# Performance work log

Measured on AMD Instinct MI355X. Metric: run time of the kernel, lower is better.

## Reference

```python
import jax, jax.numpy as jnp
import numpy as np

H = 512

def setup_inputs() -> dict:
    key = jax.random.key(0)
    ks = jax.random.split(key, 8)
    s = 1.0 / np.sqrt(H)
    return {
        "encoder_outputs": jax.random.normal(ks[0], (64, 2048, H), dtype=jnp.float32),
        "decoder_hidden": jax.random.normal(ks[1], (64, H), dtype=jnp.float32),
        "W1": jax.random.uniform(ks[2], (H, H), jnp.float32, -s, s),
        "b1": jax.random.uniform(ks[3], (H,), jnp.float32, -s, s),
        "W2": jax.random.uniform(ks[4], (H, H), jnp.float32, -s, s),
        "b2": jax.random.uniform(ks[5], (H,), jnp.float32, -s, s),
        "V": jax.random.uniform(ks[6], (H,), jnp.float32, -s, s),  # V weight (1, H) squeezed
        "bv": jax.random.uniform(ks[7], (1,), jnp.float32, -s, s),
    }

def reference(encoder_outputs, decoder_hidden, W1, b1, W2, b2, V, bv):
    # proj of encoder outputs: [B,S,H]; proj of decoder hidden: [B,1,H]
    enc_proj = jnp.einsum('bsh,oh->bso', encoder_outputs, W1) + b1
    dec_proj = (jnp.einsum('bh,oh->bo', decoder_hidden, W2) + b2)[:, None, :]
    energy = jnp.tanh(enc_proj + dec_proj)                      # [B,S,H]
    scores = jnp.einsum('bsh,h->bs', energy, V) + bv[0]          # [B,S]
    attn = jax.nn.softmax(scores, axis=1)                        # [B,S]
    context = jnp.einsum('bs,bsh->bh', attn, encoder_outputs)    # [B,H]
    return context, attn
```

## Files before the change

### kernel.cpp

```cpp
#include <hip/hip_runtime.h>
#include <hip/hip_bf16.h>

typedef __attribute__((ext_vector_type(4))) float f32x4;
typedef __attribute__((ext_vector_type(8))) short s16x8;
typedef __attribute__((ext_vector_type(4))) unsigned short u16x4;
typedef __attribute__((ext_vector_type(8))) __bf16 bf16x8;

#define HDIM 512
#define SEQ  2048
#define NB   64
#define BM   64
#define NBLK ((NB * SEQ) / BM)
#define CPB  (SEQ / BM)

static __device__ __forceinline__ unsigned short f2bf(float f) {
  unsigned u = __float_as_uint(f);
  u += 0x7fffu + ((u >> 16) & 1u);
  return (unsigned short)(u >> 16);
}
static __device__ __forceinline__ float bf2f(unsigned short v) {
  return __uint_as_float(((unsigned)v) << 16);
}

static __device__ __forceinline__ f32x4 mfma16(s16x8 a, s16x8 b, f32x4 c) {
  return __builtin_amdgcn_mfma_f32_16x16x32_bf16(
      __builtin_bit_cast(bf16x8, a), __builtin_bit_cast(bf16x8, b), c, 0, 0, 0);
}

#define BLOADG(dst, sp)                                                        \
  do {                                                                         \
    asm volatile("global_load_dwordx4 %0, %1, %2 offset:0"                     \
                 : "=&v"((dst)[0]) : "v"(voff), "s"(sp));                      \
    asm volatile("global_load_dwordx4 %0, %1, %2 offset:1024"                  \
                 : "=&v"((dst)[1]) : "v"(voff), "s"(sp));                      \
    asm volatile("global_load_dwordx4 %0, %1, %2 offset:2048"                  \
                 : "=&v"((dst)[2]) : "v"(voff), "s"(sp));                      \
    asm volatile("global_load_dwordx4 %0, %1, %2 offset:3072"                  \
                 : "=&v"((dst)[3]) : "v"(voff), "s"(sp));                      \
  } while (0)

__global__ void convert_w1(const float* __restrict__ w1,
                           unsigned short* __restrict__ o) {
  int id = blockIdx.x * 256 + threadIdx.x;
  int kk = id >> 11, n = (id >> 2) & 511, r4 = id & 3;
  const float* src = w1 + (long)n * HDIM + kk * 32 + r4 * 8;
  f32x4 v0 = *(const f32x4*)src;
  f32x4 v1 = *(const f32x4*)(src + 4);
  u16x4 a, b;
  a.x = f2bf(v0.x); a.y = f2bf(v0.y); a.z = f2bf(v0.z); a.w = f2bf(v0.w);
  b.x = f2bf(v1.x); b.y = f2bf(v1.y); b.z = f2bf(v1.z); b.w = f2bf(v1.w);
  unsigned short* dst = o + (long)id * 8;
  *(u16x4*)dst = a;
  *(u16x4*)(dst + 4) = b;
}

__global__ void zproj(const float* __restrict__ dec, const float* __restrict__ W2,
                      const float* __restrict__ b1, const float* __restrict__ b2,
                      float* __restrict__ zfull) {
  int b = blockIdx.x, oc = blockIdx.y, tid = threadIdx.x;
  int o = oc * 256 + tid;
  __shared__ float d_s[HDIM];
  d_s[tid] = dec[b * HDIM + tid];
  d_s[tid + 256] = dec[b * HDIM + tid + 256];
  __syncthreads();
  const float* w = W2 + (long)o * HDIM;
  float s = 0.f;
#pragma unroll 4
  for (int k = 0; k < HDIM; k += 4) {
    f32x4 v = *(const f32x4*)(w + k);
    s += v.x * d_s[k] + v.y * d_s[k + 1] + v.z * d_s[k + 2] + v.w * d_s[k + 3];
  }
  zfull[b * HDIM + o] = s + b1[o] + b2[o];
}

__global__ __launch_bounds__(512, 4)
void gemm_fused(const float* __restrict__ enc, const unsigned short* __restrict__ w1k,
                const float* __restrict__ zfull, const float* __restrict__ V,
                const float* __restrict__ bv, float* __restrict__ scores,
                unsigned short* __restrict__ pctx, float* __restrict__ ml) {
  __shared__ __align__(16) char pool[71936];
  unsigned short* Asm = (unsigned short*)pool;
  float* zbuf = (float*)(pool + 65536);
  float* vbuf = (float*)(pool + 67584);
  float* red  = (float*)(pool + 69632);
  float* plds = (float*)(pool + 71680);
  float* pcr  = (float*)pool;

  const int tid = threadIdx.x;
  const int wid = tid >> 6;
  const int lane = tid & 63;
  const long m0 = (long)blockIdx.x * BM;
  const int b = (int)(m0 >> 11);

  zbuf[tid] = zfull[b * HDIM + tid];
  vbuf[tid] = V[tid];

  {
    const float* Ablk = enc + m0 * HDIM;
    const int qf32 = tid & 127;
    const int rbase = tid >> 7;
    const int q = qf32 >> 1, half = qf32 & 1;
#pragma unroll
    for (int j = 0; j < 16; ++j) {
      const int row = j * 4 + rbase;
      f32x4 v = *(const f32x4*)(Ablk + (long)row * HDIM + qf32 * 4);
      u16x4 pk;
      pk.x = f2bf(v.x); pk.y = f2bf(v.y); pk.z = f2bf(v.z); pk.w = f2bf(v.w);
      *(u16x4*)((char*)Asm + row * 1024 + ((q ^ (row & 7)) * 16) + half * 8) = pk;
    }
  }

  const int r4 = lane >> 4, c15 = lane & 15, c7 = c15 & 7;
  const char* Ab = (const char*)Asm;
  const unsigned voff = (unsigned)((wid * 64 + c15) * 64 + r4 * 16);
  const int widu = __builtin_amdgcn_readfirstlane(wid);

  f32x4 acc[4][4] = {};
  s16x8 bX[4], bY[4];

  __syncthreads();

  BLOADG(bX, w1k + ((widu & 15) * 16384));

#pragma unroll
  for (int kk = 0; kk < 16; ++kk) {
    const int ke = (kk + widu) & 15;
    s16x8* cur = (kk & 1) ? bY : bX;
    s16x8* nxt = (kk & 1) ? bX : bY;

    s16x8 af[4];
    const int abase = c15 * 1024 + (((ke * 4 + r4) ^ c7) * 16);
#pragma unroll
    for (int mf = 0; mf < 4; ++mf)
      af[mf] = *(const s16x8*)(Ab + abase + mf * 16384);

    if (kk < 15) {
      const unsigned short* sp = w1k + ((((kk + 1) + widu) & 15) * 16384);
      BLOADG(nxt, sp);
      asm volatile("s_waitcnt vmcnt(4)");
    } else {
      asm volatile("s_waitcnt vmcnt(0)");
    }
    __builtin_amdgcn_sched_barrier(0);

#pragma unroll
    for (int mf = 0; mf < 4; ++mf)
#pragma unroll
      for (int nf = 0; nf < 4; ++nf)
        acc[mf][nf] = mfma16(af[mf], cur[nf], acc[mf][nf]);
  }

  float zr[4], vr[4];
#pragma unroll
  for (int nf = 0; nf < 4; ++nf) {
    const int n = wid * 64 + nf * 16 + c15;
    zr[nf] = zbuf[n];
    vr[nf] = vbuf[n];
  }
#pragma unroll
  for (int mf = 0; mf < 4; ++mf) {
#pragma unroll
    for (int j = 0; j < 4; ++j) {
      float s = 0.f;
#pragma unroll
      for (int nf = 0; nf < 4; ++nf) {
        float x = acc[mf][nf][j] + zr[nf];
        float e = __expf(2.f * x);
        float t = 1.f - 2.f * __builtin_amdgcn_rcpf(e + 1.f);
        s += t * vr[nf];
      }
      s += __shfl_xor(s, 1); s += __shfl_xor(s, 2);
      s += __shfl_xor(s, 4); s += __shfl_xor(s, 8);
      if (c15 == 0) red[wid * BM + mf * 16 + r4 * 4 + j] = s;
    }
  }
  __syncthreads();

  if (tid < BM) {
    float s = 0.f;
#pragma unroll
    for (int w = 0; w < 8; ++w) s += red[w * BM + tid];
    s += bv[0];
    scores[m0 + tid] = s;
    float mc = s;
#pragma unroll
    for (int off = 1; off < 64; off <<= 1) mc = fmaxf(mc, __shfl_xor(mc, off));
    float p = __expf(s - mc);
    plds[tid] = p;
    float lc = p;
#pragma unroll
    for (int off = 1; off < 64; off <<= 1) lc += __shfl_xor(lc, off);
    if (tid == 0) { ml[blockIdx.x * 2] = mc; ml[blockIdx.x * 2 + 1] = lc; }
  }
  __syncthreads();

  float c8[8] = {};
#pragma unroll
  for (int rr = 0; rr < 8; ++rr) {
    const int r = wid * 8 + rr;
    s16x8 v = *(const s16x8*)(Ab + r * 1024 + ((lane ^ rr) * 16));
    const float p = plds[r];
#pragma unroll
    for (int e = 0; e < 8; ++e)
      c8[e] += p * bf2f((unsigned short)v[e]);
  }
  __syncthreads();
  {
    f32x4 w0, w1;
    w0.x = c8[0]; w0.y = c8[1]; w0.z = c8[2]; w0.w = c8[3];
    w1.x = c8[4]; w1.y = c8[5]; w1.z = c8[6]; w1.w = c8[7];
    *(f32x4*)((char*)pcr + wid * 2048 + lane * 32) = w0;
    *(f32x4*)((char*)pcr + wid * 2048 + lane * 32 + 16) = w1;
  }
  __syncthreads();
  {
    float s = 0.f;
#pragma unroll
    for (int g = 0; g < 8; ++g) s += pcr[g * 512 + tid];
    pctx[(long)blockIdx.x * HDIM + tid] = f2bf(s);
  }
}

__global__ void combine(float* __restrict__ attn, const unsigned short* __restrict__ pctx,
                        const float* __restrict__ ml, float* __restrict__ ctx) {
  const int b = blockIdx.x, tid = threadIdx.x;
  const int lane = tid & 63;
  float m = -1e30f, l = 0.f;
  if (lane < CPB) {
    m = ml[(b * CPB + lane) * 2];
    l = ml[(b * CPB + lane) * 2 + 1];
  }
  float M = m;
#pragma unroll
  for (int off = 1; off < 64; off <<= 1) M = fmaxf(M, __shfl_xor(M, off));
  float le = (lane < CPB) ? l * __expf(m - M) : 0.f;
  float L = le;
#pragma unroll
  for (int off = 1; off < 64; off <<= 1) L += __shfl_xor(L, off);
  const float invL = 1.f / L;

  __shared__ float wc[CPB];
  if (tid < CPB) wc[tid] = __expf(ml[(b * CPB + tid) * 2] - M) * invL;

  float sv[4];
#pragma unroll
  for (int i = 0; i < 4; ++i) sv[i] = attn[(long)b * SEQ + i * 512 + tid];
#pragma unroll
  for (int i = 0; i < 4; ++i)
    attn[(long)b * SEQ + i * 512 + tid] = __expf(sv[i] - M) * invL;

  __syncthreads();
  float a = 0.f;
#pragma unroll 8
  for (int c = 0; c < CPB; ++c)
    a += bf2f(pctx[(long)(b * CPB + c) * HDIM + tid]) * wc[c];
  ctx[(long)b * HDIM + tid] = a;
}

extern "C" void kernel_launch(void* const* d_in, const int* in_sizes, int n_in,
                              void* d_out, int out_size, void* d_ws, size_t ws_size,
                              hipStream_t stream) {
  const float* enc = (const float*)d_in[0];
  const float* dec = (const float*)d_in[1];
  const float* W1  = (const float*)d_in[2];
  const float* b1  = (const float*)d_in[3];
  const float* W2  = (const float*)d_in[4];
  const float* b2  = (const float*)d_in[5];
  const float* V   = (const float*)d_in[6];
  const float* bv  = (const float*)d_in[7];

  float* out  = (float*)d_out;
  float* ctx  = out;
  float* attn = out + NB * HDIM;

  char* ws = (char*)d_ws;
  unsigned short* w1k  = (unsigned short*)ws;
  float*          zful = (float*)(ws + 524288);
  unsigned short* pctx = (unsigned short*)(ws + 655360);
  float*          mlb  = (float*)(ws + 2752512);
  (void)in_sizes; (void)n_in; (void)out_size; (void)ws_size;

  convert_w1<<<128, 256, 0, stream>>>(W1, w1k);
  zproj<<<dim3(NB, 2), 256, 0, stream>>>(dec, W2, b1, b2, zful);
  gemm_fused<<<NBLK, 512, 0, stream>>>(enc, w1k, zful, V, bv, attn, pctx, mlb);
  combine<<<NB, 512, 0, stream>>>(attn, pctx, mlb, ctx);
}
```

Baseline: 123.9 us.

## Stream encoder tile into LDS per k-slice, overlapped with W1 loads and MFMA

The block no longer loads and converts the whole 64x512 encoder tile to bf16 in LDS before the GEMM starts. It preloads three k-slices, then inside the k-loop issues global loads for slice kk+4 alongside the W1 fragment loads and packs slice kk+3 into LDS, with a barrier each iteration. This hides the encoder-tile load latency behind MFMA work. It also drops the per-wave staggered k order, raises wave priority around the MFMA section, and adds a workgroup barrier on every k-step.

```diff
diff --git a/kernel.cpp b/kernel.cpp
--- a/kernel.cpp
+++ b/kernel.cpp
@@ -37,6 +37,19 @@
                  : "=&v"((dst)[2]) : "v"(voff), "s"(sp));                      \
     asm volatile("global_load_dwordx4 %0, %1, %2 offset:3072"                  \
                  : "=&v"((dst)[3]) : "v"(voff), "s"(sp));                      \
+  } while (0)
+
+#define SLOAD(dst, s)                                                          \
+  asm volatile("global_load_dwordx4 %0, %1, %2"                                \
+               : "=&v"(dst) : "v"(aoff), "s"(encblk + (s) * 32))
+
+#define PACKW(src, s)                                                          \
+  do {                                                                         \
+    u16x4 pk;                                                                  \
+    pk.x = f2bf((src).x); pk.y = f2bf((src).y);                                \
+    pk.z = f2bf((src).z); pk.w = f2bf((src).w);                                \
+    *(u16x4*)((char*)Asm + wrow * 1024 +                                       \
+              (((((s) * 4) + (wc >> 1)) ^ wr7) * 16) + (wc & 1) * 8) = pk;     \
   } while (0)
 
 __global__ void convert_w1(const float* __restrict__ w1,
@@ -95,59 +108,64 @@
   zbuf[tid] = zfull[b * HDIM + tid];
   vbuf[tid] = V[tid];
 
-  {
-    const float* Ablk = enc + m0 * HDIM;
-    const int qf32 = tid & 127;
-    const int rbase = tid >> 7;
-    const int q = qf32 >> 1, half = qf32 & 1;
-#pragma unroll
-    for (int j = 0; j < 16; ++j) {
-      const int row = j * 4 + rbase;
-      f32x4 v = *(const f32x4*)(Ablk + (long)row * HDIM + qf32 * 4);
-      u16x4 pk;
-      pk.x = f2bf(v.x); pk.y = f2bf(v.y); pk.z = f2bf(v.z); pk.w = f2bf(v.w);
-      *(u16x4*)((char*)Asm + row * 1024 + ((q ^ (row & 7)) * 16) + half * 8) = pk;
-    }
-  }
-
   const int r4 = lane >> 4, c15 = lane & 15, c7 = c15 & 7;
   const char* Ab = (const char*)Asm;
   const unsigned voff = (unsigned)((wid * 64 + c15) * 64 + r4 * 16);
-  const int widu = __builtin_amdgcn_readfirstlane(wid);
+
+  const int wrow = tid >> 3, wc = tid & 7, wr7 = wrow & 7;
+  const float* encblk = enc + m0 * HDIM;
+  const unsigned aoff = (unsigned)(wrow * 2048 + wc * 16);
+
+  {
+    const float* ep = encblk + (long)wrow * HDIM + wc * 4;
+#pragma unroll
+    for (int s = 0; s < 3; ++s) {
+      f32x4 v = *(const f32x4*)(ep + s * 32);
+      PACKW(v, s);
+    }
+  }
+  __syncthreads();
 
   f32x4 acc[4][4] = {};
   s16x8 bX[4], bY[4];
-
-  __syncthreads();
-
-  BLOADG(bX, w1k + ((widu & 15) * 16384));
+  f32x4 sb0, sb1;
+
+  SLOAD(sb1, 3);
+  BLOADG(bX, w1k);
 
 #pragma unroll
   for (int kk = 0; kk < 16; ++kk) {
-    const int ke = (kk + widu) & 15;
-    s16x8* cur = (kk & 1) ? bY : bX;
-    s16x8* nxt = (kk & 1) ? bX : bY;
-
-    s16x8 af[4];
-    const int abase = c15 * 1024 + (((ke * 4 + r4) ^ c7) * 16);
-#pragma unroll
-    for (int mf = 0; mf < 4; ++mf)
-      af[mf] = *(const s16x8*)(Ab + abase + mf * 16384);
-
-    if (kk < 15) {
-      const unsigned short* sp = w1k + ((((kk + 1) + widu) & 15) * 16384);
-      BLOADG(nxt, sp);
-      asm volatile("s_waitcnt vmcnt(4)");
-    } else {
-      asm volatile("s_waitcnt vmcnt(0)");
-    }
+    if (kk <= 11) {
+      if (kk & 1) SLOAD(sb1, kk + 4); else SLOAD(sb0, kk + 4);
+    }
+    if (kk <= 14) {
+      const unsigned short* sp = w1k + (kk + 1) * 16384;
+      if (kk & 1) BLOADG(bX, sp); else BLOADG(bY, sp);
+    }
+    if (kk <= 11)      asm volatile("s_waitcnt vmcnt(5)" ::: "memory");
+    else if (kk <= 14) asm volatile("s_waitcnt vmcnt(4)" ::: "memory");
+    else               asm volatile("s_waitcnt vmcnt(0)" ::: "memory");
     __builtin_amdgcn_sched_barrier(0);
-
-#pragma unroll
-    for (int mf = 0; mf < 4; ++mf)
-#pragma unroll
-      for (int nf = 0; nf < 4; ++nf)
-        acc[mf][nf] = mfma16(af[mf], cur[nf], acc[mf][nf]);
+    if (kk <= 12) {
+      if (kk & 1) PACKW(sb0, kk + 3); else PACKW(sb1, kk + 3);
+    }
+    asm volatile("s_waitcnt lgkmcnt(0)" ::: "memory");
+    __builtin_amdgcn_s_barrier();
+    __builtin_amdgcn_sched_barrier(0);
+    const int abase = c15 * 1024 + (((kk * 4 + r4) ^ c7) * 16);
+    __builtin_amdgcn_s_setprio(1);
+#pragma unroll
+    for (int mf = 0; mf < 4; ++mf) {
+      s16x8 af = *(const s16x8*)(Ab + abase + mf * 16384);
+      if (kk & 1) {
+#pragma unroll
+        for (int nf = 0; nf < 4; ++nf) acc[mf][nf] = mfma16(af, bY[nf], acc[mf][nf]);
+      } else {
+#pragma unroll
+        for (int nf = 0; nf < 4; ++nf) acc[mf][nf] = mfma16(af, bX[nf], acc[mf][nf]);
+      }
+    }
+    __builtin_amdgcn_s_setprio(0);
   }
 
   float zr[4], vr[4];
```

Measured after the change: 125.0 us. Within noise of the previous version (+0.9%).

## Merge prep kernels, pipeline A-tile staging, and split MFMA waits per B fragment

Applied to the files above, without the earlier changes.

Combines the W1 conversion and decoder projection into one launch to save a kernel launch. The encoder tile staging now issues batches of inline-asm global loads and overlaps them with bf16 packing into shared memory, instead of doing loads and packs in sequence. The main loop waits for each B fragment separately, so MFMAs on early fragments can start before the later loads land, and it raises wave priority around the MFMA section. The z and V vectors are now read straight from global memory instead of staged LDS buffers, which shrinks LDS use but adds scattered global reads in the epilogue.

```diff
diff --git a/kernel.cpp b/kernel.cpp
--- a/kernel.cpp
+++ b/kernel.cpp
@@ -39,38 +39,59 @@
                  : "=&v"((dst)[3]) : "v"(voff), "s"(sp));                      \
   } while (0)
 
-__global__ void convert_w1(const float* __restrict__ w1,
-                           unsigned short* __restrict__ o) {
-  int id = blockIdx.x * 256 + threadIdx.x;
-  int kk = id >> 11, n = (id >> 2) & 511, r4 = id & 3;
-  const float* src = w1 + (long)n * HDIM + kk * 32 + r4 * 8;
-  f32x4 v0 = *(const f32x4*)src;
-  f32x4 v1 = *(const f32x4*)(src + 4);
-  u16x4 a, b;
-  a.x = f2bf(v0.x); a.y = f2bf(v0.y); a.z = f2bf(v0.z); a.w = f2bf(v0.w);
-  b.x = f2bf(v1.x); b.y = f2bf(v1.y); b.z = f2bf(v1.z); b.w = f2bf(v1.w);
-  unsigned short* dst = o + (long)id * 8;
-  *(u16x4*)dst = a;
-  *(u16x4*)(dst + 4) = b;
-}
-
-__global__ void zproj(const float* __restrict__ dec, const float* __restrict__ W2,
-                      const float* __restrict__ b1, const float* __restrict__ b2,
-                      float* __restrict__ zfull) {
-  int b = blockIdx.x, oc = blockIdx.y, tid = threadIdx.x;
-  int o = oc * 256 + tid;
-  __shared__ float d_s[HDIM];
-  d_s[tid] = dec[b * HDIM + tid];
-  d_s[tid + 256] = dec[b * HDIM + tid + 256];
-  __syncthreads();
-  const float* w = W2 + (long)o * HDIM;
-  float s = 0.f;
+#define SLOAD(dst, s)                                                          \
+  asm volatile("global_load_dwordx4 %0, %1, %2"                                \
+               : "=&v"(dst) : "v"(aoff), "s"(encblk + (s) * 32))
+
+#define WAITV(N)                                                               \
+  do {                                                                         \
+    asm volatile("s_waitcnt vmcnt(%0)" :: "i"(N) : "memory");                  \
+    __builtin_amdgcn_sched_barrier(0);                                         \
+  } while (0)
+
+#define PACKW(src, s)                                                          \
+  do {                                                                         \
+    u16x4 pk;                                                                  \
+    pk.x = f2bf((src).x); pk.y = f2bf((src).y);                                \
+    pk.z = f2bf((src).z); pk.w = f2bf((src).w);                                \
+    *(u16x4*)((char*)Asm + wrow * 1024 +                                       \
+              (((((s) * 4) + (wc >> 1)) ^ wr7) * 16) + (wc & 1) * 8) = pk;     \
+  } while (0)
+
+__global__ void prep(const float* __restrict__ w1, unsigned short* __restrict__ o,
+                     const float* __restrict__ dec, const float* __restrict__ W2,
+                     const float* __restrict__ b1, const float* __restrict__ b2,
+                     float* __restrict__ zfull) {
+  const int bx = blockIdx.x, tid = threadIdx.x;
+  if (bx < 128) {
+    int id = bx * 256 + tid;
+    int kk = id >> 11, n = (id >> 2) & 511, r4 = id & 3;
+    const float* src = w1 + (long)n * HDIM + kk * 32 + r4 * 8;
+    f32x4 v0 = *(const f32x4*)src;
+    f32x4 v1 = *(const f32x4*)(src + 4);
+    u16x4 a, b;
+    a.x = f2bf(v0.x); a.y = f2bf(v0.y); a.z = f2bf(v0.z); a.w = f2bf(v0.w);
+    b.x = f2bf(v1.x); b.y = f2bf(v1.y); b.z = f2bf(v1.z); b.w = f2bf(v1.w);
+    unsigned short* dst = o + (long)id * 8;
+    *(u16x4*)dst = a;
+    *(u16x4*)(dst + 4) = b;
+  } else {
+    const int idx = bx - 128;
+    const int b = idx >> 1, oc = idx & 1;
+    const int oo = oc * 256 + tid;
+    __shared__ float d_s[HDIM];
+    d_s[tid] = dec[b * HDIM + tid];
+    d_s[tid + 256] = dec[b * HDIM + tid + 256];
+    __syncthreads();
+    const float* w = W2 + (long)oo * HDIM;
+    float s = 0.f;
 #pragma unroll 4
-  for (int k = 0; k < HDIM; k += 4) {
-    f32x4 v = *(const f32x4*)(w + k);
-    s += v.x * d_s[k] + v.y * d_s[k + 1] + v.z * d_s[k + 2] + v.w * d_s[k + 3];
-  }
-  zfull[b * HDIM + o] = s + b1[o] + b2[o];
+    for (int k = 0; k < HDIM; k += 4) {
+      f32x4 v = *(const f32x4*)(w + k);
+      s += v.x * d_s[k] + v.y * d_s[k + 1] + v.z * d_s[k + 2] + v.w * d_s[k + 3];
+    }
+    zfull[b * HDIM + oo] = s + b1[oo] + b2[oo];
+  }
 }
 
 __global__ __launch_bounds__(512, 4)
@@ -78,12 +99,10 @@
                 const float* __restrict__ zfull, const float* __restrict__ V,
                 const float* __restrict__ bv, float* __restrict__ scores,
                 unsigned short* __restrict__ pctx, float* __restrict__ ml) {
-  __shared__ __align__(16) char pool[71936];
+  __shared__ __align__(16) char pool[67840];
   unsigned short* Asm = (unsigned short*)pool;
-  float* zbuf = (float*)(pool + 65536);
-  float* vbuf = (float*)(pool + 67584);
-  float* red  = (float*)(pool + 69632);
-  float* plds = (float*)(pool + 71680);
+  float* red  = (float*)(pool + 65536);
+  float* plds = (float*)(pool + 67584);
   float* pcr  = (float*)pool;
 
   const int tid = threadIdx.x;
@@ -92,33 +111,34 @@
   const long m0 = (long)blockIdx.x * BM;
   const int b = (int)(m0 >> 11);
 
-  zbuf[tid] = zfull[b * HDIM + tid];
-  vbuf[tid] = V[tid];
-
-  {
-    const float* Ablk = enc + m0 * HDIM;
-    const int qf32 = tid & 127;
-    const int rbase = tid >> 7;
-    const int q = qf32 >> 1, half = qf32 & 1;
-#pragma unroll
-    for (int j = 0; j < 16; ++j) {
-      const int row = j * 4 + rbase;
-      f32x4 v = *(const f32x4*)(Ablk + (long)row * HDIM + qf32 * 4);
-      u16x4 pk;
-      pk.x = f2bf(v.x); pk.y = f2bf(v.y); pk.z = f2bf(v.z); pk.w = f2bf(v.w);
-      *(u16x4*)((char*)Asm + row * 1024 + ((q ^ (row & 7)) * 16) + half * 8) = pk;
-    }
-  }
-
   const int r4 = lane >> 4, c15 = lane & 15, c7 = c15 & 7;
   const char* Ab = (const char*)Asm;
   const unsigned voff = (unsigned)((wid * 64 + c15) * 64 + r4 * 16);
   const int widu = __builtin_amdgcn_readfirstlane(wid);
 
+  const int wrow = tid >> 3, wc = tid & 7, wr7 = wrow & 7;
+  const float* encblk = enc + m0 * HDIM;
+  const unsigned aoff = (unsigned)(wrow * 2048 + wc * 16);
+
+  {
+    f32x4 pa, pb, pc, pd, pe, pf, pg, ph;
+    SLOAD(pa, 0); SLOAD(pb, 1); SLOAD(pc, 2); SLOAD(pd, 3);
+    SLOAD(pe, 4); SLOAD(pf, 5); SLOAD(pg, 6); SLOAD(ph, 7);
+    WAITV(4);
+    PACKW(pa, 0); PACKW(pb, 1); PACKW(pc, 2); PACKW(pd, 3);
+    SLOAD(pa, 8); SLOAD(pb, 9); SLOAD(pc, 10); SLOAD(pd, 11);
+    WAITV(4);
+    PACKW(pe, 4); PACKW(pf, 5); PACKW(pg, 6); PACKW(ph, 7);
+    SLOAD(pe, 12); SLOAD(pf, 13); SLOAD(pg, 14); SLOAD(ph, 15);
+    WAITV(4);
+    PACKW(pa, 8); PACKW(pb, 9); PACKW(pc, 10); PACKW(pd, 11);
+    WAITV(0);
+    PACKW(pe, 12); PACKW(pf, 13); PACKW(pg, 14); PACKW(ph, 15);
+  }
+  __syncthreads();
+
   f32x4 acc[4][4] = {};
   s16x8 bX[4], bY[4];
-
-  __syncthreads();
 
   BLOADG(bX, w1k + ((widu & 15) * 16384));
 
@@ -134,28 +154,46 @@
     for (int mf = 0; mf < 4; ++mf)
       af[mf] = *(const s16x8*)(Ab + abase + mf * 16384);
 
+    if (kk < 15)
+      BLOADG(nxt, w1k + ((((kk + 1) + widu) & 15) * 16384));
+
+    __builtin_amdgcn_s_setprio(1);
     if (kk < 15) {
-      const unsigned short* sp = w1k + ((((kk + 1) + widu) & 15) * 16384);
-      BLOADG(nxt, sp);
-      asm volatile("s_waitcnt vmcnt(4)");
+      WAITV(7);
+#pragma unroll
+      for (int mf = 0; mf < 4; ++mf) acc[mf][0] = mfma16(af[mf], cur[0], acc[mf][0]);
+      WAITV(6);
+#pragma unroll
+      for (int mf = 0; mf < 4; ++mf) acc[mf][1] = mfma16(af[mf], cur[1], acc[mf][1]);
+      WAITV(5);
+#pragma unroll
+      for (int mf = 0; mf < 4; ++mf) acc[mf][2] = mfma16(af[mf], cur[2], acc[mf][2]);
+      WAITV(4);
+#pragma unroll
+      for (int mf = 0; mf < 4; ++mf) acc[mf][3] = mfma16(af[mf], cur[3], acc[mf][3]);
     } else {
-      asm volatile("s_waitcnt vmcnt(0)");
+      WAITV(3);
+#pragma unroll
+      for (int mf = 0; mf < 4; ++mf) acc[mf][0] = mfma16(af[mf], cur[0], acc[mf][0]);
+      WAITV(2);
+#pragma unroll
+      for (int mf = 0; mf < 4; ++mf) acc[mf][1] = mfma16(af[mf], cur[1], acc[mf][1]);
+      WAITV(1);
+#pragma unroll
+      for (int mf = 0; mf < 4; ++mf) acc[mf][2] = mfma16(af[mf], cur[2], acc[mf][2]);
+      WAITV(0);
+#pragma unroll
+      for (int mf = 0; mf < 4; ++mf) acc[mf][3] = mfma16(af[mf], cur[3], acc[mf][3]);
     }
-    __builtin_amdgcn_sched_barrier(0);
-
-#pragma unroll
-    for (int mf = 0; mf < 4; ++mf)
-#pragma unroll
-      for (int nf = 0; nf < 4; ++nf)
-        acc[mf][nf] = mfma16(af[mf], cur[nf], acc[mf][nf]);
+    __builtin_amdgcn_s_setprio(0);
   }
 
   float zr[4], vr[4];
 #pragma unroll
   for (int nf = 0; nf < 4; ++nf) {
     const int n = wid * 64 + nf * 16 + c15;
-    zr[nf] = zbuf[n];
-    vr[nf] = vbuf[n];
+    zr[nf] = zfull[b * HDIM + n];
+    vr[nf] = V[n];
   }
 #pragma unroll
   for (int mf = 0; mf < 4; ++mf) {
@@ -280,8 +318,7 @@
   float*          mlb  = (float*)(ws + 2752512);
   (void)in_sizes; (void)n_in; (void)out_size; (void)ws_size;
 
-  convert_w1<<<128, 256, 0, stream>>>(W1, w1k);
-  zproj<<<dim3(NB, 2), 256, 0, stream>>>(dec, W2, b1, b2, zful);
+  prep<<<256, 256, 0, stream>>>(W1, w1k, dec, W2, b1, b2, zful);
   gemm_fused<<<NBLK, 512, 0, stream>>>(enc, w1k, zful, V, bv, attn, pctx, mlb);
   combine<<<NB, 512, 0, stream>>>(attn, pctx, mlb, ctx);
 }
```

Measured after the change: 118.1 us. 4.7% less time.
